# Kernel tuning notes

Measured on AMD Instinct MI355X. Metric: run time of the kernel, lower is better.

Reference implementation:

```python
import jax, jax.numpy as jnp
import numpy as np

KH, KW = 3, 3          # kernel_size
SH, SW = 2, 2          # strides
OUT_CH = 16            # num_channels
CD0, CD1 = 4, 4        # capsule_dim
ROUTING_ITER = 3


def _extract_blocks(x, kh, kw, sh, sw):
    """x: [B, H, W, ...trailing] -> [B, oh, ow, kh, kw, ...trailing] (VALID padding)."""
    B, H, W = x.shape[:3]
    oh = (H - kh) // sh + 1
    ow = (W - kw) // sw + 1
    rows = []
    for i in range(kh):
        cols = []
        for j in range(kw):
            cols.append(x[:, i:i + oh * sh:sh, j:j + ow * sw:sw])
        rows.append(jnp.stack(cols, axis=3))          # [B,oh,ow,kw,...]
    return jnp.stack(rows, axis=3)                    # [B,oh,ow,kh,kw,...]


def _squash(s, eps=1e-9):
    # squash over the last two (pose-matrix) axes
    sq = jnp.sum(s * s, axis=(-2, -1), keepdims=True)
    return s * (sq / (1.0 + sq)) / jnp.sqrt(sq + eps)


def setup_inputs() -> dict:
    key = jax.random.key(0)
    k1, k2, k3 = jax.random.split(key, 3)
    input_poses = jax.random.normal(k1, (8, 32, 32, 16, CD0, CD1), dtype=jnp.float32)
    input_activations = jax.random.uniform(k2, (8, 32, 32, 16), dtype=jnp.float32)
    # he_normal for the 4x4 transform matrices: fan_in ~ CD1
    std = np.sqrt(2.0 / CD1).astype(np.float32)
    kernel = std * jax.random.normal(k3, (OUT_CH, KH, KW, 16, CD0, CD1), dtype=jnp.float32)
    return {"input_poses": input_poses,
            "input_activations": input_activations,
            "kernel": kernel}


def reference(input_poses, input_activations, kernel):
    # input_poses: [B,H,W,Cin,4,4]; kernel: [O,kh,kw,Cin,4,4]
    blocks = _extract_blocks(input_poses, KH, KW, SH, SW)  # [B,oh,ow,kh,kw,Cin,4,4]
    # votes: pose @ W per (output channel, kernel pos, input channel)
    votes = jnp.einsum('bhwklcpq,oklcqr->bhwoklcpr', blocks, kernel)
    B, oh, ow = votes.shape[:3]
    cin = blocks.shape[5]
    N = KH * KW * cin  # votes per output capsule
    votes = votes.reshape(B, oh, ow, OUT_CH, N, CD0, CD1)

    # dynamic routing (Sabour et al.): softmax of coupling logits over output channels
    b = jnp.zeros((B, oh, ow, OUT_CH, N), dtype=votes.dtype)
    v = None
    for _ in range(ROUTING_ITER):
        c = jax.nn.softmax(b, axis=3)                              # over output capsules
        s = jnp.einsum('bhwon,bhwonpq->bhwopq', c, votes)          # weighted vote sum
        v = _squash(s)                                             # [B,oh,ow,O,4,4]
        b = b + jnp.einsum('bhwopq,bhwonpq->bhwon', v, votes)      # agreement update

    capsule_poses = v
    # activation == 'norm': length of the (already squashed) capsule vector
    capsule_activations = jnp.sqrt(
        jnp.sum(capsule_poses * capsule_poses, axis=(-2, -1)) + 1e-12)
    return capsule_poses, capsule_activations
```

## Files before the change

kernel.cpp:

```cpp
#include <hip/hip_runtime.h>


#define OH 15
#define OW 15
#define N_VOTES 144
#define VPT 9
#define POSE_PAD 20
#define B_PAD 17

__global__ __launch_bounds__(256, 2)
void convcaps_routing_kernel(const float* __restrict__ poses,
                             const float* __restrict__ kern,
                             float* __restrict__ out)
{
    __shared__ float pose_lds[N_VOTES * POSE_PAD];
    __shared__ float b_lds[N_VOTES * B_PAD];
    __shared__ float nmax[N_VOTES];
    __shared__ float rden[N_VOTES];

    const int site = blockIdx.x;
    const int b    = site / (OH * OW);
    const int rem  = site % (OH * OW);
    const int h    = rem / OW;
    const int w    = rem % OW;

    const int t  = threadIdx.x;
    const int o  = t >> 4;
    const int nt = t & 15;

    const float* pbase = poses + (size_t)b * (32 * 32 * 256);
    for (int idx = t; idx < N_VOTES * 4; idx += 256) {
        int n  = idx >> 2;
        int e4 = idx & 3;
        int kl = n >> 4;
        int c  = n & 15;
        int k  = kl / 3, l = kl % 3;
        int y  = 2 * h + k, x = 2 * w + l;
        const float4 v = *reinterpret_cast<const float4*>(
            pbase + (size_t)(y * 32 + x) * 256 + c * 16 + e4 * 4);
        *reinterpret_cast<float4*>(&pose_lds[n * POSE_PAD + e4 * 4]) = v;
    }
    __syncthreads();

    float vreg[VPT][16];
    #pragma unroll
    for (int j = 0; j < VPT; ++j) {
        const int n = nt + 16 * j;
        const float* Kp = kern + ((size_t)(o * N_VOTES + n) << 4);
        const float4 k0 = reinterpret_cast<const float4*>(Kp)[0];
        const float4 k1 = reinterpret_cast<const float4*>(Kp)[1];
        const float4 k2 = reinterpret_cast<const float4*>(Kp)[2];
        const float4 k3 = reinterpret_cast<const float4*>(Kp)[3];
        const float* P = &pose_lds[n * POSE_PAD];
        #pragma unroll
        for (int p = 0; p < 4; ++p) {
            const float p0 = P[p * 4 + 0], p1 = P[p * 4 + 1];
            const float p2 = P[p * 4 + 2], p3 = P[p * 4 + 3];
            vreg[j][p * 4 + 0] = p0 * k0.x + p1 * k1.x + p2 * k2.x + p3 * k3.x;
            vreg[j][p * 4 + 1] = p0 * k0.y + p1 * k1.y + p2 * k2.y + p3 * k3.y;
            vreg[j][p * 4 + 2] = p0 * k0.z + p1 * k1.z + p2 * k2.z + p3 * k3.z;
            vreg[j][p * 4 + 3] = p0 * k0.w + p1 * k1.w + p2 * k2.w + p3 * k3.w;
        }
    }

    float breg[VPT];
    #pragma unroll
    for (int j = 0; j < VPT; ++j) breg[j] = 0.0f;

    float vfin[16];

    #pragma unroll
    for (int iter = 0; iter < 3; ++iter) {
        float c_[VPT];
        if (iter == 0) {
            #pragma unroll
            for (int j = 0; j < VPT; ++j) c_[j] = 1.0f / 16.0f;
        } else {
            #pragma unroll
            for (int j = 0; j < VPT; ++j) {
                const int n = nt + 16 * j;
                c_[j] = __expf(breg[j] - nmax[n]) * rden[n];
            }
        }

        float s[16];
        #pragma unroll
        for (int e = 0; e < 16; ++e) s[e] = 0.0f;
        #pragma unroll
        for (int j = 0; j < VPT; ++j) {
            #pragma unroll
            for (int e = 0; e < 16; ++e) s[e] += c_[j] * vreg[j][e];
        }
        #pragma unroll
        for (int m = 1; m <= 8; m <<= 1) {
            #pragma unroll
            for (int e = 0; e < 16; ++e) s[e] += __shfl_xor(s[e], m, 64);
        }

        float sq = 0.0f;
        #pragma unroll
        for (int e = 0; e < 16; ++e) sq += s[e] * s[e];
        const float factor = (sq / (1.0f + sq)) * rsqrtf(sq + 1e-9f);
        #pragma unroll
        for (int e = 0; e < 16; ++e) vfin[e] = s[e] * factor;

        if (iter < 2) {
            #pragma unroll
            for (int j = 0; j < VPT; ++j) {
                float d = 0.0f;
                #pragma unroll
                for (int e = 0; e < 16; ++e) d += vfin[e] * vreg[j][e];
                breg[j] += d;
                b_lds[(nt + 16 * j) * B_PAD + o] = breg[j];
            }
            __syncthreads();
            if (t < N_VOTES) {
                float mx = -1e30f;
                #pragma unroll
                for (int oo = 0; oo < 16; ++oo)
                    mx = fmaxf(mx, b_lds[t * B_PAD + oo]);
                float sum = 0.0f;
                #pragma unroll
                for (int oo = 0; oo < 16; ++oo)
                    sum += __expf(b_lds[t * B_PAD + oo] - mx);
                nmax[t] = mx;
                rden[t] = 1.0f / sum;
            }
            __syncthreads();
        }
    }

    float vout = vfin[0];
    #pragma unroll
    for (int e = 1; e < 16; ++e) {
        if (nt == e) vout = vfin[e];
    }
    out[(size_t)site * 256 + t] = vout;

    if (nt == 0) {
        float sqv = 0.0f;
        #pragma unroll
        for (int e = 0; e < 16; ++e) sqv += vfin[e] * vfin[e];
        out[460800 + (size_t)site * 16 + o] = sqrtf(sqv + 1e-12f);
    }
}

extern "C" void kernel_launch(void* const* d_in, const int* in_sizes, int n_in,
                              void* d_out, int out_size, void* d_ws, size_t ws_size,
                              hipStream_t stream) {
    const float* poses = (const float*)d_in[0];
    const float* kern  = (const float*)d_in[2];
    float* outp = (float*)d_out;

    convcaps_routing_kernel<<<dim3(8 * OH * OW), dim3(256), 0, stream>>>(
        poses, kern, outp);
}
```

Measured before the change: 45.07 us.

## Split each output capsule's votes across 32 lanes with 512-thread blocks

After: 81.13 us. +80.0%, slower.

```diff
diff --git a/kernel.cpp b/kernel.cpp
--- a/kernel.cpp
+++ b/kernel.cpp
@@ -4,11 +4,11 @@
 #define OH 15
 #define OW 15
 #define N_VOTES 144
-#define VPT 9
+#define VPT 5
 #define POSE_PAD 20
 #define B_PAD 17
 
-__global__ __launch_bounds__(256, 2)
+__global__ __launch_bounds__(512, 4)
 void convcaps_routing_kernel(const float* __restrict__ poses,
                              const float* __restrict__ kern,
                              float* __restrict__ out)
@@ -25,11 +25,11 @@
     const int w    = rem % OW;
 
     const int t  = threadIdx.x;
-    const int o  = t >> 4;
-    const int nt = t & 15;
+    const int o  = t >> 5;
+    const int nt = t & 31;
 
     const float* pbase = poses + (size_t)b * (32 * 32 * 256);
-    for (int idx = t; idx < N_VOTES * 4; idx += 256) {
+    for (int idx = t; idx < N_VOTES * 4; idx += 512) {
         int n  = idx >> 2;
         int e4 = idx & 3;
         int kl = n >> 4;
@@ -45,21 +45,27 @@
     float vreg[VPT][16];
     #pragma unroll
     for (int j = 0; j < VPT; ++j) {
-        const int n = nt + 16 * j;
-        const float* Kp = kern + ((size_t)(o * N_VOTES + n) << 4);
-        const float4 k0 = reinterpret_cast<const float4*>(Kp)[0];
-        const float4 k1 = reinterpret_cast<const float4*>(Kp)[1];
-        const float4 k2 = reinterpret_cast<const float4*>(Kp)[2];
-        const float4 k3 = reinterpret_cast<const float4*>(Kp)[3];
-        const float* P = &pose_lds[n * POSE_PAD];
-        #pragma unroll
-        for (int p = 0; p < 4; ++p) {
-            const float p0 = P[p * 4 + 0], p1 = P[p * 4 + 1];
-            const float p2 = P[p * 4 + 2], p3 = P[p * 4 + 3];
-            vreg[j][p * 4 + 0] = p0 * k0.x + p1 * k1.x + p2 * k2.x + p3 * k3.x;
-            vreg[j][p * 4 + 1] = p0 * k0.y + p1 * k1.y + p2 * k2.y + p3 * k3.y;
-            vreg[j][p * 4 + 2] = p0 * k0.z + p1 * k1.z + p2 * k2.z + p3 * k3.z;
-            vreg[j][p * 4 + 3] = p0 * k0.w + p1 * k1.w + p2 * k2.w + p3 * k3.w;
+        const int n = nt + 32 * j;
+        const bool real = (j < 4) || (nt < 16);
+        if (real) {
+            const float* Kp = kern + ((size_t)(o * N_VOTES + n) << 4);
+            const float4 k0 = reinterpret_cast<const float4*>(Kp)[0];
+            const float4 k1 = reinterpret_cast<const float4*>(Kp)[1];
+            const float4 k2 = reinterpret_cast<const float4*>(Kp)[2];
+            const float4 k3 = reinterpret_cast<const float4*>(Kp)[3];
+            const float* P = &pose_lds[n * POSE_PAD];
+            #pragma unroll
+            for (int p = 0; p < 4; ++p) {
+                const float p0 = P[p * 4 + 0], p1 = P[p * 4 + 1];
+                const float p2 = P[p * 4 + 2], p3 = P[p * 4 + 3];
+                vreg[j][p * 4 + 0] = p0 * k0.x + p1 * k1.x + p2 * k2.x + p3 * k3.x;
+                vreg[j][p * 4 + 1] = p0 * k0.y + p1 * k1.y + p2 * k2.y + p3 * k3.y;
+                vreg[j][p * 4 + 2] = p0 * k0.z + p1 * k1.z + p2 * k2.z + p3 * k3.z;
+                vreg[j][p * 4 + 3] = p0 * k0.w + p1 * k1.w + p2 * k2.w + p3 * k3.w;
+            }
+        } else {
+            #pragma unroll
+            for (int e = 0; e < 16; ++e) vreg[j][e] = 0.0f;
         }
     }
 
@@ -67,32 +73,24 @@
     #pragma unroll
     for (int j = 0; j < VPT; ++j) breg[j] = 0.0f;
 
-    float vfin[16];
+    float s[16];
 
     #pragma unroll
     for (int iter = 0; iter < 3; ++iter) {
-        float c_[VPT];
-        if (iter == 0) {
-            #pragma unroll
-            for (int j = 0; j < VPT; ++j) c_[j] = 1.0f / 16.0f;
-        } else {
-            #pragma unroll
-            for (int j = 0; j < VPT; ++j) {
-                const int n = nt + 16 * j;
-                c_[j] = __expf(breg[j] - nmax[n]) * rden[n];
-            }
-        }
-
-        float s[16];
         #pragma unroll
         for (int e = 0; e < 16; ++e) s[e] = 0.0f;
         #pragma unroll
         for (int j = 0; j < VPT; ++j) {
+            const int n = nt + 32 * j;
+            const bool real = (j < 4) || (nt < 16);
+            float c;
+            if (iter == 0) c = 1.0f / 16.0f;
+            else           c = real ? __expf(breg[j] - nmax[n]) * rden[n] : 0.0f;
             #pragma unroll
-            for (int e = 0; e < 16; ++e) s[e] += c_[j] * vreg[j][e];
+            for (int e = 0; e < 16; ++e) s[e] += c * vreg[j][e];
         }
         #pragma unroll
-        for (int m = 1; m <= 8; m <<= 1) {
+        for (int m = 1; m <= 16; m <<= 1) {
             #pragma unroll
             for (int e = 0; e < 16; ++e) s[e] += __shfl_xor(s[e], m, 64);
         }
@@ -102,16 +100,18 @@
         for (int e = 0; e < 16; ++e) sq += s[e] * s[e];
         const float factor = (sq / (1.0f + sq)) * rsqrtf(sq + 1e-9f);
         #pragma unroll
-        for (int e = 0; e < 16; ++e) vfin[e] = s[e] * factor;
+        for (int e = 0; e < 16; ++e) s[e] *= factor;
 
         if (iter < 2) {
             #pragma unroll
             for (int j = 0; j < VPT; ++j) {
                 float d = 0.0f;
                 #pragma unroll
-                for (int e = 0; e < 16; ++e) d += vfin[e] * vreg[j][e];
+                for (int e = 0; e < 16; ++e) d += s[e] * vreg[j][e];
                 breg[j] += d;
-                b_lds[(nt + 16 * j) * B_PAD + o] = breg[j];
+                const int n = nt + 32 * j;
+                const bool real = (j < 4) || (nt < 16);
+                if (real) b_lds[n * B_PAD + o] = breg[j];
             }
             __syncthreads();
             if (t < N_VOTES) {
@@ -130,17 +130,17 @@
         }
     }
 
-    float vout = vfin[0];
-    #pragma unroll
-    for (int e = 1; e < 16; ++e) {
-        if (nt == e) vout = vfin[e];
-    }
-    out[(size_t)site * 256 + t] = vout;
-
-    if (nt == 0) {
+    if (nt < 16) {
+        float vout = s[0];
+        #pragma unroll
+        for (int e = 1; e < 16; ++e) {
+            if (nt == e) vout = s[e];
+        }
+        out[(size_t)site * 256 + o * 16 + nt] = vout;
+    } else if (nt == 16) {
         float sqv = 0.0f;
         #pragma unroll
-        for (int e = 0; e < 16; ++e) sqv += vfin[e] * vfin[e];
+        for (int e = 0; e < 16; ++e) sqv += s[e] * s[e];
         out[460800 + (size_t)site * 16 + o] = sqrtf(sqv + 1e-12f);
     }
 }
@@ -152,6 +152,6 @@
     const float* kern  = (const float*)d_in[2];
     float* outp = (float*)d_out;
 
-    convcaps_routing_kernel<<<dim3(8 * OH * OW), dim3(256), 0, stream>>>(
+    convcaps_routing_kernel<<<dim3(8 * OH * OW), dim3(512), 0, stream>>>(
         poses, kern, outp);
 }
```

## Pack routing votes as bf16 pairs in registers to raise occupancy

Applied to the files above, without the earlier changes.

New measurement: 175.4 us. 289% more time.

```diff
diff --git a/kernel.cpp b/kernel.cpp
--- a/kernel.cpp
+++ b/kernel.cpp
@@ -8,7 +8,14 @@
 #define POSE_PAD 20
 #define B_PAD 17
 
-__global__ __launch_bounds__(256, 2)
+__device__ __forceinline__ float bf_lo(unsigned int pk) {
+    return __uint_as_float(pk << 16);
+}
+__device__ __forceinline__ float bf_hi(unsigned int pk) {
+    return __uint_as_float(pk & 0xffff0000u);
+}
+
+__global__ __launch_bounds__(256, 3)
 void convcaps_routing_kernel(const float* __restrict__ poses,
                              const float* __restrict__ kern,
                              float* __restrict__ out)
@@ -42,7 +49,7 @@
     }
     __syncthreads();
 
-    float vreg[VPT][16];
+    unsigned int vregp[VPT][8];
     #pragma unroll
     for (int j = 0; j < VPT; ++j) {
         const int n = nt + 16 * j;
@@ -52,14 +59,22 @@
         const float4 k2 = reinterpret_cast<const float4*>(Kp)[2];
         const float4 k3 = reinterpret_cast<const float4*>(Kp)[3];
         const float* P = &pose_lds[n * POSE_PAD];
+        float ve[16];
         #pragma unroll
         for (int p = 0; p < 4; ++p) {
             const float p0 = P[p * 4 + 0], p1 = P[p * 4 + 1];
             const float p2 = P[p * 4 + 2], p3 = P[p * 4 + 3];
-            vreg[j][p * 4 + 0] = p0 * k0.x + p1 * k1.x + p2 * k2.x + p3 * k3.x;
-            vreg[j][p * 4 + 1] = p0 * k0.y + p1 * k1.y + p2 * k2.y + p3 * k3.y;
-            vreg[j][p * 4 + 2] = p0 * k0.z + p1 * k1.z + p2 * k2.z + p3 * k3.z;
-            vreg[j][p * 4 + 3] = p0 * k0.w + p1 * k1.w + p2 * k2.w + p3 * k3.w;
+            ve[p * 4 + 0] = p0 * k0.x + p1 * k1.x + p2 * k2.x + p3 * k3.x;
+            ve[p * 4 + 1] = p0 * k0.y + p1 * k1.y + p2 * k2.y + p3 * k3.y;
+            ve[p * 4 + 2] = p0 * k0.z + p1 * k1.z + p2 * k2.z + p3 * k3.z;
+            ve[p * 4 + 3] = p0 * k0.w + p1 * k1.w + p2 * k2.w + p3 * k3.w;
+        }
+        #pragma unroll
+        for (int pr = 0; pr < 8; ++pr) {
+            unsigned int pk;
+            asm("v_cvt_pk_bf16_f32 %0, %1, %2"
+                : "=v"(pk) : "v"(ve[2 * pr]), "v"(ve[2 * pr + 1]));
+            vregp[j][pr] = pk;
         }
     }
 
@@ -67,29 +82,26 @@
     #pragma unroll
     for (int j = 0; j < VPT; ++j) breg[j] = 0.0f;
 
-    float vfin[16];
+    float s[16];
 
     #pragma unroll
     for (int iter = 0; iter < 3; ++iter) {
-        float c_[VPT];
-        if (iter == 0) {
-            #pragma unroll
-            for (int j = 0; j < VPT; ++j) c_[j] = 1.0f / 16.0f;
-        } else {
-            #pragma unroll
-            for (int j = 0; j < VPT; ++j) {
-                const int n = nt + 16 * j;
-                c_[j] = __expf(breg[j] - nmax[n]) * rden[n];
-            }
-        }
-
-        float s[16];
         #pragma unroll
         for (int e = 0; e < 16; ++e) s[e] = 0.0f;
         #pragma unroll
         for (int j = 0; j < VPT; ++j) {
+            float c;
+            if (iter == 0) c = 1.0f / 16.0f;
+            else {
+                const int n = nt + 16 * j;
+                c = __expf(breg[j] - nmax[n]) * rden[n];
+            }
             #pragma unroll
-            for (int e = 0; e < 16; ++e) s[e] += c_[j] * vreg[j][e];
+            for (int pr = 0; pr < 8; ++pr) {
+                const unsigned int pk = vregp[j][pr];
+                s[2 * pr + 0] += c * bf_lo(pk);
+                s[2 * pr + 1] += c * bf_hi(pk);
+            }
         }
         #pragma unroll
         for (int m = 1; m <= 8; m <<= 1) {
@@ -102,14 +114,18 @@
         for (int e = 0; e < 16; ++e) sq += s[e] * s[e];
         const float factor = (sq / (1.0f + sq)) * rsqrtf(sq + 1e-9f);
         #pragma unroll
-        for (int e = 0; e < 16; ++e) vfin[e] = s[e] * factor;
+        for (int e = 0; e < 16; ++e) s[e] *= factor;
 
         if (iter < 2) {
             #pragma unroll
             for (int j = 0; j < VPT; ++j) {
                 float d = 0.0f;
                 #pragma unroll
-                for (int e = 0; e < 16; ++e) d += vfin[e] * vreg[j][e];
+                for (int pr = 0; pr < 8; ++pr) {
+                    const unsigned int pk = vregp[j][pr];
+                    d += s[2 * pr + 0] * bf_lo(pk);
+                    d += s[2 * pr + 1] * bf_hi(pk);
+                }
                 breg[j] += d;
                 b_lds[(nt + 16 * j) * B_PAD + o] = breg[j];
             }
@@ -130,17 +146,17 @@
         }
     }
 
-    float vout = vfin[0];
+    float vout = s[0];
     #pragma unroll
     for (int e = 1; e < 16; ++e) {
-        if (nt == e) vout = vfin[e];
+        if (nt == e) vout = s[e];
     }
     out[(size_t)site * 256 + t] = vout;
 
     if (nt == 0) {
         float sqv = 0.0f;
         #pragma unroll
-        for (int e = 0; e < 16; ++e) sqv += vfin[e] * vfin[e];
+        for (int e = 0; e < 16; ++e) sqv += s[e] * s[e];
         out[460800 + (size_t)site * 16 + o] = sqrtf(sqv + 1e-12f);
     }
 }
```
